# Kernel optimization log

Measured on AMD Instinct MI355X. Metric: run time of the kernel, lower is better.

## Reference

```python
import jax, jax.numpy as jnp
import numpy as np

BS = 8192
NUM_CLASSES = 400
D = 768


def _bilin_from_14(m14, Y, X, eH, eW):
    # Value of bilinear-resize(m14 -> (eH,eW)) at integer pixel (Y,X), computed on the fly.
    # torch F.interpolate(align_corners=False): src = (dst+0.5)*in/out - 0.5, clamped at 0.
    # m14: (bs,14,14); Y,X: (bs,14) float integer-valued coords; eH,eW: (bs,) float.
    sy = jnp.maximum((Y + 0.5) * 14.0 / eH[:, None] - 0.5, 0.0)
    sx = jnp.maximum((X + 0.5) * 14.0 / eW[:, None] - 0.5, 0.0)
    r0f = jnp.floor(sy); c0f = jnp.floor(sx)
    r0 = r0f.astype(jnp.int32); r1 = jnp.minimum(r0 + 1, 13)
    c0 = c0f.astype(jnp.int32); c1 = jnp.minimum(c0 + 1, 13)
    fy = sy - r0f; fx = sx - c0f
    b = jnp.arange(m14.shape[0])[:, None, None]
    g00 = m14[b, r0[:, :, None], c0[:, None, :]]
    g01 = m14[b, r0[:, :, None], c1[:, None, :]]
    g10 = m14[b, r1[:, :, None], c0[:, None, :]]
    g11 = m14[b, r1[:, :, None], c1[:, None, :]]
    wy = fy[:, :, None]; wx = fx[:, None, :]
    return g00 * (1 - wy) * (1 - wx) + g01 * (1 - wy) * wx + g10 * wy * (1 - wx) + g11 * wy * wx


def _get_mask(attn, o_pos, e_pos):
    # Fused, fully-batched equivalent of the per-sample python loop:
    #   resize 14x14 -> (eH,eW) bilinear; crop (top,left,oH,oW); resize -> 14x14 bilinear.
    # The final resize only reads the intermediate grid at 4 integer points per output
    # pixel, so we evaluate those points lazily via _bilin_from_14 (exact, no Emax grid).
    bs = attn.shape[0]
    m14 = attn.reshape(bs, 14, 14)
    eH = e_pos[:, 2].astype(jnp.float32); eW = e_pos[:, 3].astype(jnp.float32)
    top = (o_pos[:, 0] - e_pos[:, 0]).astype(jnp.float32)
    left = (o_pos[:, 1] - e_pos[:, 1]).astype(jnp.float32)
    oH = o_pos[:, 2].astype(jnp.float32); oW = o_pos[:, 3].astype(jnp.float32)
    i = jnp.arange(14, dtype=jnp.float32)[None, :]
    ty = jnp.maximum((i + 0.5) * oH[:, None] / 14.0 - 0.5, 0.0)  # (bs,14) coords in crop
    tx = jnp.maximum((i + 0.5) * oW[:, None] / 14.0 - 0.5, 0.0)
    y0 = jnp.floor(ty); y1 = jnp.minimum(y0 + 1.0, oH[:, None] - 1.0); wy = ty - y0
    x0 = jnp.floor(tx); x1 = jnp.minimum(x0 + 1.0, oW[:, None] - 1.0); wx = tx - x0
    Y0 = top[:, None] + y0; Y1 = top[:, None] + y1  # absolute rows in (eH,eW) grid
    X0 = left[:, None] + x0; X1 = left[:, None] + x1
    v00 = _bilin_from_14(m14, Y0, X0, eH, eW)
    v01 = _bilin_from_14(m14, Y0, X1, eH, eW)
    v10 = _bilin_from_14(m14, Y1, X0, eH, eW)
    v11 = _bilin_from_14(m14, Y1, X1, eH, eW)
    wyc = wy[:, :, None]; wxc = wx[:, None, :]
    out = v00 * (1 - wyc) * (1 - wxc) + v01 * (1 - wyc) * wxc + v10 * wyc * (1 - wxc) + v11 * wyc * wxc
    return out.reshape(bs, 196)


def _get_att_mask(attention, ratio=0.5):
    bs = attention.shape[0]
    a14 = attention.reshape(bs, 14, 14)
    # bilinear 14->7 with align_corners=False samples at frac 0.5 == 2x2 average pool
    a7 = a14.reshape(bs, 7, 2, 7, 2).mean(axis=(2, 4))
    flat = a7.reshape(bs, 49)
    n_keep = int(49 * ratio) + 1  # argsort desc, take top N+1 = 25
    _, idx = jax.lax.top_k(flat, n_keep)
    masks = jnp.ones((bs, 49), dtype=bool)
    masks = masks.at[jnp.arange(bs)[:, None], idx].set(False)
    m7 = masks.reshape(bs, 7, 7)
    full = jnp.repeat(jnp.repeat(m7, 2, axis=1), 2, axis=2)
    return full.reshape(bs, 196)


def setup_inputs() -> dict:
    key = jax.random.key(0)
    k1, k2, k3 = jax.random.split(key, 3)
    attn = jax.random.uniform(k1, (BS, 196), dtype=jnp.float32)
    rng = np.random.default_rng(0)
    IMG = 224
    eH = rng.integers(112, IMG + 1, BS); eW = rng.integers(112, IMG + 1, BS)
    eT = rng.integers(0, IMG - eH + 1); eL = rng.integers(0, IMG - eW + 1)
    def box():
        h = rng.integers(56, eH + 1); w = rng.integers(56, eW + 1)
        t = eT + rng.integers(0, eH - h + 1); l = eL + rng.integers(0, eW - w + 1)
        return np.stack([t, l, h, w], axis=1)
    e = np.stack([eT, eL, eH, eW], axis=1)
    pos = np.stack([box(), box(), e], axis=1).astype(np.int32)  # (BS,3,4)
    image_embed = jax.random.normal(k2, (2 * BS, D), dtype=jnp.float32)
    W = jax.random.normal(k3, (NUM_CLASSES, D), dtype=jnp.float32) * 0.02
    b = jnp.zeros((NUM_CLASSES,), dtype=jnp.float32)
    return {"attn": attn, "pos": jnp.asarray(pos), "image_embed": image_embed, "W": W, "b": b}


def reference(attn, pos, image_embed, W, b):
    cm1 = _get_mask(attn, pos[:, 0], pos[:, 2])
    mask1 = _get_att_mask(cm1)
    cm2 = _get_mask(attn, pos[:, 1], pos[:, 2])
    mask2 = _get_att_mask(cm2)
    mask = jnp.concatenate([mask1, mask2], axis=0)  # (2*bs,196) bool, fed to masked encoder
    logits = image_embed @ W.T + b
    return logits, mask
```

## Files before the change

kernel.cpp:

```cpp
#include <hip/hip_runtime.h>
#include <hip/hip_bf16.h>
#include <stdint.h>
#include <type_traits>

#define BSAMP 8192
#define NCLS 400
#define DIM 768
#define LOGITS_SIZE (16384LL * 400LL)
#define GEMM_BLOCKS 1280
#define MASK_BLOCKS 4096
#define W_ELEMS (NCLS * DIM)

typedef __attribute__((ext_vector_type(8))) short short8;
typedef __attribute__((ext_vector_type(4))) float floatx4;

__device__ inline unsigned int packbf(float a, float b) {
    unsigned int ua = __float_as_uint(a) + 0x8000u;
    unsigned int ub = __float_as_uint(b) + 0x8000u;
    return __builtin_amdgcn_perm(ub, ua, 0x07060302u);
}

__device__ inline short8 cvt8(float4 lo, float4 hi) {
    union { unsigned int u[4]; short8 s; } r;
    r.u[0] = packbf(lo.x, lo.y);
    r.u[1] = packbf(lo.z, lo.w);
    r.u[2] = packbf(hi.x, hi.y);
    r.u[3] = packbf(hi.z, hi.w);
    return r.s;
}

__device__ inline void gload16(const void* g, void* l) {
    __builtin_amdgcn_global_load_lds((const __attribute__((address_space(1))) void*)g,
                                     (__attribute__((address_space(3))) void*)l, 16, 0, 0);
}

__global__ void cvtW_kernel(const float* __restrict__ W, unsigned short* __restrict__ ws) {
    int i = (blockIdx.x * 256 + threadIdx.x) * 4;
    if (i < W_ELEMS) {
        float4 f = *(const float4*)(W + i);
        uint2 r;
        r.x = packbf(f.x, f.y);
        r.y = packbf(f.z, f.w);
        *(uint2*)(ws + i) = r;
    }
}

__device__ inline float tap4(const float* m14, int r0, int c0, float fy, float fx) {
    int r1 = min(r0 + 1, 13);
    int c1 = min(c0 + 1, 13);
    float g00 = m14[r0 * 14 + c0];
    float g01 = m14[r0 * 14 + c1];
    float g10 = m14[r1 * 14 + c0];
    float g11 = m14[r1 * 14 + c1];
    return g00 * (1.f - fy) * (1.f - fx) + g01 * (1.f - fy) * fx +
           g10 * fy * (1.f - fx) + g11 * fy * fx;
}

struct MaskSm { float m14[4][208]; float a7[4][56]; float mv[4][56]; };

template <bool USE_WS>
struct GemmSm {
    float A[2][64 * 32];
    typename std::conditional<USE_WS, unsigned short, float>::type B[2][80 * 32];
};

template <bool USE_WS>
__global__ __launch_bounds__(256, 6) void fused_kernel(const float* __restrict__ attn,
                                                       const int* __restrict__ pos,
                                                       const float* __restrict__ E,
                                                       const float* __restrict__ W,
                                                       const float* __restrict__ bias,
                                                       const unsigned short* __restrict__ wsW,
                                                       float* __restrict__ out) {
    __shared__ __align__(16) union SmU {
        GemmSm<USE_WS> g;
        MaskSm m;
    } sm;

    const int bx = blockIdx.x;
    const int t  = threadIdx.x;
    const int wv = t >> 6, ln = t & 63;

    if (bx < GEMM_BLOCKS) {
        const int xcd = bx & 7;
        const int j   = bx >> 3;
        const int n0  = (j % 5) * 80;
        const int m0  = (xcd * 32 + j / 5) * 64;
        const int quad = ln >> 4, l16 = ln & 15;

        auto stageA = [&](int k0, float* buf) {
#pragma unroll
            for (int jj = 0; jj < 2; ++jj) {
                int r = wv * 16 + jj * 8 + (ln >> 3);
                int c = ln & 7;
                const float* src = E + (size_t)(m0 + r) * DIM + k0 + 4 * (c ^ (r & 7));
                gload16(src, buf + (wv * 16 + jj * 8) * 32);
            }
        };
        auto stageBw = [&](int k0, unsigned short* buf) {
            for (int jj = wv; jj < 5; jj += 4) {
                int row = jj * 16 + (ln >> 2);
                int c = ln & 3;
                const unsigned short* src = wsW + (size_t)(n0 + row) * DIM + k0 + 8 * (c ^ ((row >> 1) & 3));
                gload16(src, buf + (jj * 16) * 32);
            }
        };
        auto stageBf = [&](int k0, float* buf) {
            for (int jj = wv; jj < 10; jj += 4) {
                int r = jj * 8 + (ln >> 3);
                int c = ln & 7;
                const float* src = W + (size_t)(n0 + r) * DIM + k0 + 4 * (c ^ (r & 7));
                gload16(src, buf + (jj * 8) * 32);
            }
        };
        auto stage = [&](int k0, int buf) {
            stageA(k0, sm.g.A[buf]);
            if constexpr (USE_WS) stageBw(k0, sm.g.B[buf]);
            else stageBf(k0, (float*)sm.g.B[buf]);
        };

        floatx4 acc[5];
#pragma unroll
        for (int ni = 0; ni < 5; ++ni) acc[ni] = (floatx4){0.f, 0.f, 0.f, 0.f};

        stage(0, 0);
        stage(32, 1);
        __syncthreads();

        for (int it = 0; it < 24; ++it) {
            const int cur = it & 1;

            short8 af;
            {
                int rx = l16 & 7;
                const float* rp = sm.g.A[cur] + (wv * 16 + l16) * 32;
                float4 lo = *(const float4*)(rp + (((quad << 1) ^ rx) << 2));
                float4 hi = *(const float4*)(rp + ((((quad << 1) | 1) ^ rx) << 2));
                af = cvt8(lo, hi);
            }
#pragma unroll
            for (int ni = 0; ni < 5; ++ni) {
                int row = ni * 16 + l16;
                short8 bfr;
                if constexpr (USE_WS) {
                    bfr = *(const short8*)(sm.g.B[cur] + row * 32 + 8 * (quad ^ ((row >> 1) & 3)));
                } else {
                    int rx = row & 7;
                    const float* rp = (const float*)sm.g.B[cur] + row * 32;
                    float4 lo = *(const float4*)(rp + (((quad << 1) ^ rx) << 2));
                    float4 hi = *(const float4*)(rp + ((((quad << 1) | 1) ^ rx) << 2));
                    bfr = cvt8(lo, hi);
                }
                acc[ni] = __builtin_amdgcn_mfma_f32_16x16x32_bf16(af, bfr, acc[ni], 0, 0, 0);
            }

            __syncthreads();
            if (it < 22) stage((it + 2) * 32, cur);
        }

        const int rowBase = m0 + wv * 16 + quad * 4;
#pragma unroll
        for (int ni = 0; ni < 5; ++ni) {
            int col = n0 + ni * 16 + l16;
            float bv = bias[col];
#pragma unroll
            for (int r = 0; r < 4; ++r) {
                out[(size_t)(rowBase + r) * NCLS + col] = acc[ni][r] + bv;
            }
        }
    } else {
        const int p = (bx - GEMM_BLOCKS) * 4 + wv;
        const int b = p >> 1;
        const int o = p & 1;
        float* m14 = sm.m.m14[wv];

        for (int i = ln; i < 196; i += 64) m14[i] = attn[(size_t)b * 196 + i];

        const int* pb = pos + (size_t)b * 12;
        const float topf  = (float)(pb[o * 4 + 0] - pb[8]);
        const float leftf = (float)(pb[o * 4 + 1] - pb[9]);
        const float oH = (float)pb[o * 4 + 2];
        const float oW = (float)pb[o * 4 + 3];
        const float eH = (float)pb[10];
        const float eW = (float)pb[11];
        __syncthreads();

        const int i7 = ln / 7, j7 = ln - i7 * 7;
        if (ln < 49) {
            int   cI[2][2];  float cF[2][2];  float wxs[2];
            int   rI[2][2];  float rF[2][2];  float wys[2];
#pragma unroll
            for (int dx = 0; dx < 2; ++dx) {
                int ox = 2 * j7 + dx;
                float tx = fmaxf((ox + 0.5f) * oW / 14.0f - 0.5f, 0.0f);
                float x0 = floorf(tx);
                float x1 = fminf(x0 + 1.0f, oW - 1.0f);
                wxs[dx] = tx - x0;
                float X0 = leftf + x0, X1 = leftf + x1;
                float sx0 = fmaxf((X0 + 0.5f) * 14.0f / eW - 0.5f, 0.0f);
                float c0f = floorf(sx0);
                cI[dx][0] = (int)c0f; cF[dx][0] = sx0 - c0f;
                float sx1 = fmaxf((X1 + 0.5f) * 14.0f / eW - 0.5f, 0.0f);
                float c1f = floorf(sx1);
                cI[dx][1] = (int)c1f; cF[dx][1] = sx1 - c1f;
            }
#pragma unroll
            for (int dy = 0; dy < 2; ++dy) {
                int oy = 2 * i7 + dy;
                float ty = fmaxf((oy + 0.5f) * oH / 14.0f - 0.5f, 0.0f);
                float y0 = floorf(ty);
                float y1 = fminf(y0 + 1.0f, oH - 1.0f);
                wys[dy] = ty - y0;
                float Y0 = topf + y0, Y1 = topf + y1;
                float sy0 = fmaxf((Y0 + 0.5f) * 14.0f / eH - 0.5f, 0.0f);
                float r0f = floorf(sy0);
                rI[dy][0] = (int)r0f; rF[dy][0] = sy0 - r0f;
                float sy1 = fmaxf((Y1 + 0.5f) * 14.0f / eH - 0.5f, 0.0f);
                float r1f = floorf(sy1);
                rI[dy][1] = (int)r1f; rF[dy][1] = sy1 - r1f;
            }

            float s = 0.f;
#pragma unroll
            for (int dy = 0; dy < 2; ++dy) {
                float wy = wys[dy];
#pragma unroll
                for (int dx = 0; dx < 2; ++dx) {
                    float wx = wxs[dx];
                    float v00 = tap4(m14, rI[dy][0], cI[dx][0], rF[dy][0], cF[dx][0]);
                    float v01 = tap4(m14, rI[dy][0], cI[dx][1], rF[dy][0], cF[dx][1]);
                    float v10 = tap4(m14, rI[dy][1], cI[dx][0], rF[dy][1], cF[dx][0]);
                    float v11 = tap4(m14, rI[dy][1], cI[dx][1], rF[dy][1], cF[dx][1]);
                    float cm = v00 * (1.f - wy) * (1.f - wx) + v01 * (1.f - wy) * wx +
                               v10 * wy * (1.f - wx) + v11 * wy * wx;
                    s += cm;
                }
            }
            sm.m.a7[wv][ln] = s * 0.25f;
        }
        __syncthreads();

        if (ln < 49) {
            float mine = sm.m.a7[wv][ln];
            int cnt = 0;
#pragma unroll 7
            for (int s2 = 0; s2 < 49; ++s2) {
                float v = sm.m.a7[wv][s2];
                cnt += (v > mine) || (v == mine && s2 < ln);
            }
            sm.m.mv[wv][ln] = (cnt < 25) ? 0.0f : 1.0f;
        }
        __syncthreads();

        float* ob = out + LOGITS_SIZE + (size_t)(o * BSAMP + b) * 196;
        for (int i = ln; i < 196; i += 64) {
            int oy = i / 14, ox = i - oy * 14;
            ob[i] = sm.m.mv[wv][(oy >> 1) * 7 + (ox >> 1)];
        }
    }
}

extern "C" void kernel_launch(void* const* d_in, const int* in_sizes, int n_in,
                              void* d_out, int out_size, void* d_ws, size_t ws_size,
                              hipStream_t stream) {
    const float* attn = (const float*)d_in[0];
    const int*   pos  = (const int*)d_in[1];
    const float* E    = (const float*)d_in[2];
    const float* W    = (const float*)d_in[3];
    const float* bias = (const float*)d_in[4];
    float* out = (float*)d_out;

    if (ws_size >= (size_t)W_ELEMS * 2) {
        unsigned short* ws = (unsigned short*)d_ws;
        cvtW_kernel<<<300, 256, 0, stream>>>(W, ws);
        fused_kernel<true><<<GEMM_BLOCKS + MASK_BLOCKS, 256, 0, stream>>>(
            attn, pos, E, W, bias, ws, out);
    } else {
        fused_kernel<false><<<GEMM_BLOCKS + MASK_BLOCKS, 256, 0, stream>>>(
            attn, pos, E, W, bias, nullptr, out);
    }
}
```

Baseline: 150.6 us.

## Double GEMM M-tile and load A directly from global into registers

Doubles the GEMM block tile from 64 to 128 rows, halving GEMM block count, with each wave computing two 16-row groups that share each B fragment. A is no longer staged through shared memory but is prefetched straight from global into registers two iterations ahead. B (bf16 weights) is staged in 128-wide K chunks split across waves, which cuts barriers from 24 to 6. The trade-offs are higher register pressure (launch bounds lowered to 4 blocks per CU), fewer blocks to spread across the GPU, and uncoalesced-style per-lane global reads of A.

```diff
diff --git a/kernel.cpp b/kernel.cpp
--- a/kernel.cpp
+++ b/kernel.cpp
@@ -7,7 +7,7 @@
 #define NCLS 400
 #define DIM 768
 #define LOGITS_SIZE (16384LL * 400LL)
-#define GEMM_BLOCKS 1280
+#define GEMM_BLOCKS 640
 #define MASK_BLOCKS 4096
 #define W_ELEMS (NCLS * DIM)
 
@@ -58,14 +58,10 @@
 
 struct MaskSm { float m14[4][208]; float a7[4][56]; float mv[4][56]; };
 
+struct GemmSm { unsigned short B[2][4][80 * 32]; };
+
 template <bool USE_WS>
-struct GemmSm {
-    float A[2][64 * 32];
-    typename std::conditional<USE_WS, unsigned short, float>::type B[2][80 * 32];
-};
-
-template <bool USE_WS>
-__global__ __launch_bounds__(256, 6) void fused_kernel(const float* __restrict__ attn,
+__global__ __launch_bounds__(256, 4) void fused_kernel(const float* __restrict__ attn,
                                                        const int* __restrict__ pos,
                                                        const float* __restrict__ E,
                                                        const float* __restrict__ W,
@@ -73,7 +69,7 @@
                                                        const unsigned short* __restrict__ wsW,
                                                        float* __restrict__ out) {
     __shared__ __align__(16) union SmU {
-        GemmSm<USE_WS> g;
+        GemmSm g;
         MaskSm m;
     } sm;
 
@@ -85,87 +81,89 @@
         const int xcd = bx & 7;
         const int j   = bx >> 3;
         const int n0  = (j % 5) * 80;
-        const int m0  = (xcd * 32 + j / 5) * 64;
+        const int m0  = (xcd * 16 + j / 5) * 128;
         const int quad = ln >> 4, l16 = ln & 15;
 
-        auto stageA = [&](int k0, float* buf) {
-#pragma unroll
-            for (int jj = 0; jj < 2; ++jj) {
-                int r = wv * 16 + jj * 8 + (ln >> 3);
-                int c = ln & 7;
-                const float* src = E + (size_t)(m0 + r) * DIM + k0 + 4 * (c ^ (r & 7));
-                gload16(src, buf + (wv * 16 + jj * 8) * 32);
-            }
-        };
-        auto stageBw = [&](int k0, unsigned short* buf) {
-            for (int jj = wv; jj < 5; jj += 4) {
-                int row = jj * 16 + (ln >> 2);
-                int c = ln & 3;
-                const unsigned short* src = wsW + (size_t)(n0 + row) * DIM + k0 + 8 * (c ^ ((row >> 1) & 3));
-                gload16(src, buf + (jj * 16) * 32);
-            }
-        };
-        auto stageBf = [&](int k0, float* buf) {
-            for (int jj = wv; jj < 10; jj += 4) {
-                int r = jj * 8 + (ln >> 3);
-                int c = ln & 7;
-                const float* src = W + (size_t)(n0 + r) * DIM + k0 + 4 * (c ^ (r & 7));
-                gload16(src, buf + (jj * 8) * 32);
-            }
-        };
-        auto stage = [&](int k0, int buf) {
-            stageA(k0, sm.g.A[buf]);
-            if constexpr (USE_WS) stageBw(k0, sm.g.B[buf]);
-            else stageBf(k0, (float*)sm.g.B[buf]);
-        };
-
-        floatx4 acc[5];
-#pragma unroll
-        for (int ni = 0; ni < 5; ++ni) acc[ni] = (floatx4){0.f, 0.f, 0.f, 0.f};
-
-        stage(0, 0);
-        stage(32, 1);
-        __syncthreads();
-
-        for (int it = 0; it < 24; ++it) {
-            const int cur = it & 1;
-
-            short8 af;
-            {
-                int rx = l16 & 7;
-                const float* rp = sm.g.A[cur] + (wv * 16 + l16) * 32;
-                float4 lo = *(const float4*)(rp + (((quad << 1) ^ rx) << 2));
-                float4 hi = *(const float4*)(rp + ((((quad << 1) | 1) ^ rx) << 2));
-                af = cvt8(lo, hi);
-            }
-#pragma unroll
-            for (int ni = 0; ni < 5; ++ni) {
-                int row = ni * 16 + l16;
-                short8 bfr;
-                if constexpr (USE_WS) {
-                    bfr = *(const short8*)(sm.g.B[cur] + row * 32 + 8 * (quad ^ ((row >> 1) & 3)));
-                } else {
-                    int rx = row & 7;
-                    const float* rp = (const float*)sm.g.B[cur] + row * 32;
-                    float4 lo = *(const float4*)(rp + (((quad << 1) ^ rx) << 2));
-                    float4 hi = *(const float4*)(rp + ((((quad << 1) | 1) ^ rx) << 2));
-                    bfr = cvt8(lo, hi);
-                }
-                acc[ni] = __builtin_amdgcn_mfma_f32_16x16x32_bf16(af, bfr, acc[ni], 0, 0, 0);
-            }
-
+        const float* aptr0 = E + (size_t)(m0 + wv * 32 + l16) * DIM + quad * 8;
+        const float* aptr1 = aptr0 + (size_t)16 * DIM;
+
+        floatx4 acc[2][5];
+#pragma unroll
+        for (int g = 0; g < 2; ++g)
+#pragma unroll
+            for (int ni = 0; ni < 5; ++ni) acc[g][ni] = (floatx4){0.f, 0.f, 0.f, 0.f};
+
+        if constexpr (USE_WS) {
+            auto stageB = [&](int s, int buf) {
+                unsigned short* dst = &sm.g.B[buf][wv][0];
+                const int rr = ln >> 2, ch = ln & 3;
+#pragma unroll
+                for (int c = 0; c < 5; ++c) {
+                    int row = c * 16 + rr;
+                    const unsigned short* src = wsW + (size_t)(n0 + row) * DIM +
+                                                s * 128 + wv * 32 + 8 * (ch ^ ((row >> 1) & 3));
+                    gload16(src, dst + c * 512);
+                }
+            };
+
+            float4 pf[2][4];
+            auto LD = [&](int it, int pb) {
+                pf[pb][0] = *(const float4*)(aptr0 + it * 32);
+                pf[pb][1] = *(const float4*)(aptr0 + it * 32 + 4);
+                pf[pb][2] = *(const float4*)(aptr1 + it * 32);
+                pf[pb][3] = *(const float4*)(aptr1 + it * 32 + 4);
+            };
+
+            stageB(0, 0);
+            LD(0, 0);
+            LD(1, 1);
             __syncthreads();
-            if (it < 22) stage((it + 2) * 32, cur);
-        }
-
-        const int rowBase = m0 + wv * 16 + quad * 4;
+
+#pragma unroll
+            for (int s = 0; s < 6; ++s) {
+                if (s < 5) stageB(s + 1, (s + 1) & 1);
+#pragma unroll
+                for (int j4 = 0; j4 < 4; ++j4) {
+                    const int it = s * 4 + j4;
+                    const int pb = it & 1;
+                    short8 af0 = cvt8(pf[pb][0], pf[pb][1]);
+                    short8 af1 = cvt8(pf[pb][2], pf[pb][3]);
+                    if (it < 22) LD(it + 2, pb);
+                    const unsigned short* bb = &sm.g.B[s & 1][j4][0];
+#pragma unroll
+                    for (int ni = 0; ni < 5; ++ni) {
+                        int row = ni * 16 + l16;
+                        short8 bfr = *(const short8*)(bb + row * 32 + 8 * (quad ^ ((row >> 1) & 3)));
+                        acc[0][ni] = __builtin_amdgcn_mfma_f32_16x16x32_bf16(af0, bfr, acc[0][ni], 0, 0, 0);
+                        acc[1][ni] = __builtin_amdgcn_mfma_f32_16x16x32_bf16(af1, bfr, acc[1][ni], 0, 0, 0);
+                    }
+                }
+                __syncthreads();
+            }
+        } else {
+#pragma unroll 4
+            for (int it = 0; it < 24; ++it) {
+                short8 af0 = cvt8(*(const float4*)(aptr0 + it * 32), *(const float4*)(aptr0 + it * 32 + 4));
+                short8 af1 = cvt8(*(const float4*)(aptr1 + it * 32), *(const float4*)(aptr1 + it * 32 + 4));
+#pragma unroll
+                for (int ni = 0; ni < 5; ++ni) {
+                    const float* wp = W + (size_t)(n0 + ni * 16 + l16) * DIM + it * 32 + quad * 8;
+                    short8 bfr = cvt8(*(const float4*)wp, *(const float4*)(wp + 4));
+                    acc[0][ni] = __builtin_amdgcn_mfma_f32_16x16x32_bf16(af0, bfr, acc[0][ni], 0, 0, 0);
+                    acc[1][ni] = __builtin_amdgcn_mfma_f32_16x16x32_bf16(af1, bfr, acc[1][ni], 0, 0, 0);
+                }
+            }
+        }
+
+        const int rowBase = m0 + wv * 32 + quad * 4;
 #pragma unroll
         for (int ni = 0; ni < 5; ++ni) {
             int col = n0 + ni * 16 + l16;
             float bv = bias[col];
 #pragma unroll
             for (int r = 0; r < 4; ++r) {
-                out[(size_t)(rowBase + r) * NCLS + col] = acc[ni][r] + bv;
+                out[(size_t)(rowBase + r) * NCLS + col]      = acc[0][ni][r] + bv;
+                out[(size_t)(rowBase + 16 + r) * NCLS + col] = acc[1][ni][r] + bv;
             }
         }
     } else {
```

Measured after the change: 150.6 us. About the same (-0.0%).
